# Performance work log

Measured on AMD Instinct MI355X. Metric: run time of the kernel, lower is better.

The kernel has to match this reference:

```python
import jax, jax.numpy as jnp
import numpy as np

# dims: O=1 templates/chains, L=384 residues, d_pair=d_bias=128, 4 heads x 32
O, L, DP, DB, H, DH = 1, 384, 128, 128, 4, 32
SCALING = 1.0 / np.sqrt(DH)


def _ln(x, g, b):
    # torch nn.LayerNorm over last dim, eps=1e-5, biased variance
    m = jnp.mean(x, axis=-1, keepdims=True)
    v = jnp.mean((x - m) ** 2, axis=-1, keepdims=True)
    return (x - m) * jax.lax.rsqrt(v + 1e-5) * g + b


def setup_inputs() -> dict:
    key = jax.random.key(0)
    ks = jax.random.split(key, 9)

    def w(k, shape, s=0.02):
        return (jax.random.normal(k, shape) * s).astype(jnp.float32)

    return {
        "pair": jax.random.normal(ks[0], (O, L, L, DP), dtype=jnp.float32),
        "bias": jax.random.normal(ks[1], (O, L, L, DB), dtype=jnp.float32),
        "ln_pair_g": jnp.ones((DP,), jnp.float32),
        "ln_pair_b": jnp.zeros((DP,), jnp.float32),
        "ln_bias_g": jnp.ones((DB,), jnp.float32),
        "ln_bias_b": jnp.zeros((DB,), jnp.float32),
        "Wq": w(ks[2], (H * DH, DP)),  # torch Linear weight layout (out, in)
        "Wk": w(ks[3], (H * DH, DP)),
        "Wv": w(ks[4], (H * DH, DP)),
        "Wb": w(ks[5], (H, DB)),
        "Wg": w(ks[6], (H * DH, DP)),
        "bg": jnp.ones((H * DH,), jnp.float32),
        "Wo": w(ks[7], (DP, H * DH)),
        "bo": w(ks[8], (DP,)),
    }


def reference(pair, bias, ln_pair_g, ln_pair_b, ln_bias_g, ln_bias_b,
              Wq, Wk, Wv, Wb, Wg, bg, Wo, bo):
    # is_row=True: swap the two L axes so attention runs along rows
    p = jnp.transpose(pair, (0, 2, 1, 3))   # [O, L, L, DP]
    bsrc = jnp.transpose(bias, (0, 2, 1, 3))  # [O, L, L, DB]

    p = _ln(p, ln_pair_g, ln_pair_b)
    bsrc = _ln(bsrc, ln_bias_g, ln_bias_b)

    q = (p @ Wq.T).reshape(O, L, L, H, DH) * SCALING
    k = (p @ Wk.T).reshape(O, L, L, H, DH) / L
    v = (p @ Wv.T).reshape(O, L, L, H, DH)
    b = bsrc @ Wb.T                         # [O, L, L, H] pairwise bias
    gate = jax.nn.sigmoid(p @ Wg.T + bg)    # [O, L, L, H*DH]

    # attention scores contracted over the non-attended axial dim n and head dim k
    attn = jnp.einsum('bnihk,bnjhk->bijh', q, k) + b
    attn = jax.nn.softmax(attn, axis=2)     # softmax over j (torch dim=-2)

    out = jnp.einsum('bijh,bnjhd->bnihd', attn, v).reshape(O, L, L, H * DH)
    out = (gate * out) @ Wo.T + bo          # [O, L, L, DP]
    return jnp.transpose(out, (0, 2, 1, 3))  # undo is_row permute
```

## Files before the change

kernel.cpp:

```cpp
#include <hip/hip_runtime.h>
#include <hip/hip_bf16.h>

#define L_DIM 384
#define DPC 128
#define NH 4
#define DHD 32
#define HD 128
#define NROWS (L_DIM*L_DIM)
#define NSPLIT 16

typedef __hip_bfloat16 bf16;
typedef __attribute__((ext_vector_type(8))) short bf8_t;
typedef __attribute__((ext_vector_type(4))) short bf4_t;
typedef __attribute__((ext_vector_type(4))) float f4_t;

__device__ __forceinline__ float bf2f(bf16 x){ return __bfloat162float(x); }
__device__ __forceinline__ bf16 f2bf(float x){ return __float2bfloat16(x); }

union bfu8 { bf8_t v; bf16 h[8]; };

__global__ __launch_bounds__(256) void k_prep(
    const float* __restrict__ Wq, const float* __restrict__ Wk, const float* __restrict__ Wv,
    const float* __restrict__ Wg, const float* __restrict__ Wo,
    bf16* __restrict__ Wqp, bf16* __restrict__ Wkp, bf16* __restrict__ Wvp,
    bf16* __restrict__ Wgp, bf16* __restrict__ Wop)
{
  const int o = blockIdx.x * 256 + threadIdx.x;
  const int j = o & 7, lane = (o >> 3) & 63, ks = (o >> 9) & 3, nt = o >> 11;
  const int src = (nt*16 + (lane & 15))*DPC + ks*32 + (lane >> 4)*8 + j;
  Wqp[o] = f2bf(Wq[src]);
  Wkp[o] = f2bf(Wk[src]);
  Wvp[o] = f2bf(Wv[src]);
  Wgp[o] = f2bf(Wg[src]);
  Wop[o] = f2bf(Wo[src]);
}

__global__ __launch_bounds__(256) void k_bias_proj(
    const float* __restrict__ bias, const float* __restrict__ lng, const float* __restrict__ lnb,
    const float* __restrict__ Wb, float* __restrict__ bscore)
{
  const int tid = threadIdx.x;
  const int wave = tid >> 6, lane = tid & 63;
  const int sub = lane >> 4, l16 = lane & 15, c = l16 * 8;
  const int t = blockIdx.x * 16 + wave * 4 + sub;
  const int j = t / L_DIM, i = t % L_DIM;

  const float4 ga = *(const float4*)&lng[c], gb = *(const float4*)&lng[c+4];
  const float4 ba = *(const float4*)&lnb[c], bb = *(const float4*)&lnb[c+4];
  const float4 xa = *(const float4*)&bias[(size_t)t * DPC + c];
  const float4 xb = *(const float4*)&bias[(size_t)t * DPC + c + 4];

  float s  = xa.x+xa.y+xa.z+xa.w + xb.x+xb.y+xb.z+xb.w;
  float ss = xa.x*xa.x+xa.y*xa.y+xa.z*xa.z+xa.w*xa.w
           + xb.x*xb.x+xb.y*xb.y+xb.z*xb.z+xb.w*xb.w;
  #pragma unroll
  for (int off = 8; off; off >>= 1) { s += __shfl_xor(s, off, 64); ss += __shfl_xor(ss, off, 64); }
  const float mean = s * (1.f/128.f);
  const float var  = ss * (1.f/128.f) - mean*mean;
  const float rstd = rsqrtf(var + 1e-5f);
  float y[8];
  y[0]=(xa.x-mean)*rstd*ga.x+ba.x; y[1]=(xa.y-mean)*rstd*ga.y+ba.y;
  y[2]=(xa.z-mean)*rstd*ga.z+ba.z; y[3]=(xa.w-mean)*rstd*ga.w+ba.w;
  y[4]=(xb.x-mean)*rstd*gb.x+bb.x; y[5]=(xb.y-mean)*rstd*gb.y+bb.y;
  y[6]=(xb.z-mean)*rstd*gb.z+bb.z; y[7]=(xb.w-mean)*rstd*gb.w+bb.w;

  float p[4];
  #pragma unroll
  for (int h = 0; h < 4; ++h) {
    const float4 wa = *(const float4*)&Wb[h*DPC + c];
    const float4 wb4 = *(const float4*)&Wb[h*DPC + c + 4];
    p[h] = y[0]*wa.x + y[1]*wa.y + y[2]*wa.z + y[3]*wa.w
         + y[4]*wb4.x + y[5]*wb4.y + y[6]*wb4.z + y[7]*wb4.w;
    #pragma unroll
    for (int off = 8; off; off >>= 1) p[h] += __shfl_xor(p[h], off, 64);
  }
  if (l16 == 0) {
    #pragma unroll
    for (int h = 0; h < 4; ++h)
      bscore[((size_t)h*L_DIM + i)*L_DIM + j] = p[h];
  }
}

__global__ __launch_bounds__(256, 6) void k_pair_proj(
    const float* __restrict__ pair, const float* __restrict__ lng, const float* __restrict__ lnb,
    const bf16* __restrict__ Wqp, const bf16* __restrict__ Wkp, const bf16* __restrict__ Wvp,
    const bf16* __restrict__ Wgp, const float* __restrict__ bg,
    bf16* __restrict__ qf, bf16* __restrict__ kf, bf16* __restrict__ vf, bf16* __restrict__ gatef)
{
  __shared__ __align__(16) bf16 Sh[4 * 3072];
  const int tid = threadIdx.x;
  const int wave = tid >> 6, lane = tid & 63;
  bf16* WS = Sh + wave * 3072;
  const int n = blockIdx.x / 6, i6 = blockIdx.x % 6;
  const int i0g = i6*64 + wave*16;
  const int m = lane & 15, q4 = lane >> 4;
  const int I = i6*4 + wave;

  {
    const int half = lane >> 5, l32 = lane & 31, c = l32 * 4;
    const float4 g4 = *(const float4*)&lng[c];
    const float4 b4 = *(const float4*)&lnb[c];
    float4 xv[8];
    #pragma unroll
    for (int rr = 0; rr < 8; ++rr)
      xv[rr] = *(const float4*)&pair[((size_t)(i0g + rr*2 + half)*L_DIM + n)*DPC + c];
    #pragma unroll
    for (int rr = 0; rr < 8; ++rr) {
      const int r = rr*2 + half;
      float s  = xv[rr].x + xv[rr].y + xv[rr].z + xv[rr].w;
      float ss = xv[rr].x*xv[rr].x + xv[rr].y*xv[rr].y + xv[rr].z*xv[rr].z + xv[rr].w*xv[rr].w;
      #pragma unroll
      for (int off = 16; off; off >>= 1) { s += __shfl_xor(s, off, 64); ss += __shfl_xor(ss, off, 64); }
      const float mean = s * (1.f/128.f);
      const float var  = ss * (1.f/128.f) - mean*mean;
      const float rstd = rsqrtf(var + 1e-5f);
      union { bf16 h[4]; bf4_t v; } pk;
      pk.h[0] = f2bf((xv[rr].x-mean)*rstd*g4.x + b4.x);
      pk.h[1] = f2bf((xv[rr].y-mean)*rstd*g4.y + b4.y);
      pk.h[2] = f2bf((xv[rr].z-mean)*rstd*g4.z + b4.z);
      pk.h[3] = f2bf((xv[rr].w-mean)*rstd*g4.w + b4.w);
      *(bf4_t*)&WS[r*136 + c] = pk.v;
    }
  }

  bf8_t afr[4];
  #pragma unroll
  for (int ks = 0; ks < 4; ++ks)
    afr[ks] = *(const bf8_t*)&WS[m*136 + ks*32 + q4*8];

  const bf16* W3[3] = {Wqp, Wkp, Wgp};
  #pragma unroll
  for (int s3 = 0; s3 < 3; ++s3) {
    const bf16* Wp = W3[s3];
    #pragma unroll
    for (int h = 0; h < 4; ++h) {
      f4_t acc0 = {0.f,0.f,0.f,0.f}, acc1 = {0.f,0.f,0.f,0.f};
      #pragma unroll
      for (int ks = 0; ks < 4; ++ks) {
        bf8_t b0 = *(const bf8_t*)&Wp[((h*2    )*4 + ks)*512 + lane*8];
        bf8_t b1 = *(const bf8_t*)&Wp[((h*2 + 1)*4 + ks)*512 + lane*8];
        acc0 = __builtin_amdgcn_mfma_f32_16x16x32_bf16(afr[ks], b0, acc0, 0, 0, 0);
        acc1 = __builtin_amdgcn_mfma_f32_16x16x32_bf16(afr[ks], b1, acc1, 0, 0, 0);
      }
      if (s3 == 2) {
        const float bg0 = bg[h*32 + m], bg1 = bg[h*32 + 16 + m];
        #pragma unroll
        for (int reg = 0; reg < 4; ++reg) {
          acc0[reg] = 1.f / (1.f + __expf(-(acc0[reg] + bg0)));
          acc1[reg] = 1.f / (1.f + __expf(-(acc1[reg] + bg1)));
        }
      }
      #pragma unroll
      for (int reg = 0; reg < 4; ++reg) {
        WS[(q4*4 + reg)*40 + m]      = f2bf(acc0[reg]);
        WS[(q4*4 + reg)*40 + 16 + m] = f2bf(acc1[reg]);
      }
      bf8_t fv = *(const bf8_t*)&WS[m*40 + q4*8];
      if (s3 == 0)
        *(bf8_t*)&qf[((((size_t)n*NH + h)*24 + I)*64 + lane)*8] = fv;
      else if (s3 == 1)
        *(bf8_t*)&kf[((((size_t)n*NH + h)*24 + I)*64 + lane)*8] = fv;
      else
        *(bf8_t*)&gatef[((((size_t)n*24 + I)*NH + h)*64 + lane)*8] = fv;
    }
  }

  #pragma unroll
  for (int nt = 0; nt < 8; ++nt) {
    f4_t acc = {0.f,0.f,0.f,0.f};
    #pragma unroll
    for (int ks = 0; ks < 4; ++ks) {
      bf8_t bfr = *(const bf8_t*)&Wvp[(nt*4 + ks)*512 + lane*8];
      acc = __builtin_amdgcn_mfma_f32_16x16x32_bf16(afr[ks], bfr, acc, 0, 0, 0);
    }
    #pragma unroll
    for (int reg = 0; reg < 4; ++reg)
      WS[(nt*16 + m)*24 + q4*4 + reg] = f2bf(acc[reg]);
  }
  const int J  = i6*2 + (wave >> 1);
  const int wo = (wave & 1) * 32;
  #pragma unroll
  for (int st = 0; st < 4; ++st) {
    const int fid = st*2 + (lane >> 5);
    const int h = fid >> 1, dt = fid & 1;
    const int lnl = lane & 31;
    bf8_t val = *(const bf8_t*)&WS[(h*32 + dt*16 + (lnl & 15))*24 + (lnl >> 4)*8];
    size_t dst = (((((size_t)n*NH + h)*12 + J)*2 + dt)*64 + (wo + lnl))*8;
    *(bf8_t*)&vf[dst] = val;
  }
}

__global__ __launch_bounds__(256) void k_qk(
    const bf16* __restrict__ qf, const bf16* __restrict__ kf, float* __restrict__ Spart)
{
  const int tid = threadIdx.x, wave = tid >> 6, lane = tid & 63;
  const int m = lane & 15, q4 = lane >> 4;
  const int b = blockIdx.x;
  const int ks = b / 36, rem = b % 36;
  const int h = rem / 9, t9 = rem % 9;
  const int i0 = (t9/3)*128, j0 = (t9%3)*128;
  const int wr = (wave >> 1)*64, wc = (wave & 1)*64;

  f4_t acc[4][4];
  #pragma unroll
  for (int a = 0; a < 4; ++a)
    #pragma unroll
    for (int c = 0; c < 4; ++c) acc[a][c] = (f4_t){0.f,0.f,0.f,0.f};

  const bf16* qp = qf + (((size_t)(ks*24)*NH + h)*24 + ((i0 + wr) >> 4))*512 + (size_t)lane*8;
  const bf16* kp = kf + (((size_t)(ks*24)*NH + h)*24 + ((j0 + wc) >> 4))*512 + (size_t)lane*8;
  const size_t nstride = (size_t)NH*24*512;

  bf8_t af[4], bfr[4];
  #pragma unroll
  for (int x = 0; x < 4; ++x) {
    af[x]  = *(const bf8_t*)(qp + x*512);
    bfr[x] = *(const bf8_t*)(kp + x*512);
  }
  #pragma unroll 2
  for (int kt = 0; kt < 24; ++kt) {
    bf8_t afn[4], bfn[4];
    if (kt < 23) {
      const bf16* qn = qp + (size_t)(kt+1)*nstride;
      const bf16* kn = kp + (size_t)(kt+1)*nstride;
      #pragma unroll
      for (int x = 0; x < 4; ++x) {
        afn[x] = *(const bf8_t*)(qn + x*512);
        bfn[x] = *(const bf8_t*)(kn + x*512);
      }
    }
    #pragma unroll
    for (int mt = 0; mt < 4; ++mt)
      #pragma unroll
      for (int nt = 0; nt < 4; ++nt)
        acc[mt][nt] = __builtin_amdgcn_mfma_f32_16x16x32_bf16(af[mt], bfr[nt], acc[mt][nt], 0, 0, 0);
    #pragma unroll
    for (int x = 0; x < 4; ++x) { af[x] = afn[x]; bfr[x] = bfn[x]; }
  }
  float* Sp = Spart + (size_t)(ks*NH + h)*L_DIM*L_DIM;
  #pragma unroll
  for (int mt = 0; mt < 4; ++mt)
    #pragma unroll
    for (int nt = 0; nt < 4; ++nt)
      #pragma unroll
      for (int reg = 0; reg < 4; ++reg) {
        int i = i0 + wr + mt*16 + q4*4 + reg;
        int j = j0 + wc + nt*16 + m;
        Sp[(size_t)i*L_DIM + j] = acc[mt][nt][reg];
      }
}

__global__ __launch_bounds__(192) void k_softmax(
    const float* __restrict__ Spart, const float* __restrict__ bscore, bf16* __restrict__ attnf)
{
  const int t = threadIdx.x, wave = t >> 6, lane = t & 63;
  const int h = blockIdx.x / L_DIM, i = blockIdx.x % L_DIM;
  const float sc = 0.17677669529663687f / 384.f;
  const size_t off = ((size_t)h*L_DIM + i)*L_DIM + t*2;

  float ax = 0.f, ay = 0.f;
  #pragma unroll
  for (int ksp = 0; ksp < NSPLIT; ++ksp) {
    float2 p = *(const float2*)&Spart[(size_t)ksp*(NH*L_DIM*L_DIM) + off];
    ax += p.x; ay += p.y;
  }
  const float2 bs = *(const float2*)&bscore[off];
  ax = ax*sc + bs.x;
  ay = ay*sc + bs.y;

  __shared__ float redm[3], reds[3];
  float mx = fmaxf(ax, ay);
  #pragma unroll
  for (int o = 32; o; o >>= 1) mx = fmaxf(mx, __shfl_xor(mx, o, 64));
  if (lane == 0) redm[wave] = mx;
  __syncthreads();
  mx = fmaxf(fmaxf(redm[0], redm[1]), redm[2]);
  float ex = __expf(ax - mx), ey = __expf(ay - mx);
  float sm = ex + ey;
  #pragma unroll
  for (int o = 32; o; o >>= 1) sm += __shfl_xor(sm, o, 64);
  if (lane == 0) reds[wave] = sm;
  __syncthreads();
  const float inv = 1.f / (reds[0] + reds[1] + reds[2]);

  const int j = t*2;
  const int I = i >> 4, mm = i & 15, J = j >> 5, q4 = (j >> 3) & 3, jj = j & 7;
  union { bf16 h2[2]; unsigned u; } pk;
  pk.h2[0] = f2bf(ex * inv);
  pk.h2[1] = f2bf(ey * inv);
  size_t a = ((((size_t)h*24 + I)*12 + J)*64 + q4*16 + mm)*8 + jj;
  *(unsigned*)&attnf[a] = pk.u;
}

__global__ __launch_bounds__(256) void k_pv(
    const bf16* __restrict__ attnf, const bf16* __restrict__ vf, const bf16* __restrict__ gatef,
    bf16* __restrict__ goutf)
{
  __shared__ __align__(16) bf16 Cs2[384*40];
  const int tid = threadIdx.x, wave = tid >> 6, lane = tid & 63;
  const int m = lane & 15, q4 = lane >> 4;
  const int n = blockIdx.x >> 2, h = blockIdx.x & 3;

  bf8_t ugp[6];
  #pragma unroll
  for (int it = 0; it < 6; ++it) {
    int u = tid + it*256;
    int I = u >> 6, ln = u & 63;
    ugp[it] = *(const bf8_t*)&gatef[((((size_t)n*24 + I)*NH + h)*64 + ln)*8];
  }

  f4_t acc[6][2];
  #pragma unroll
  for (int a = 0; a < 6; ++a) { acc[a][0] = (f4_t){0,0,0,0}; acc[a][1] = (f4_t){0,0,0,0}; }

  for (int J = 0; J < 12; ++J) {
    const bf16* vb = vf + (((size_t)(n*NH + h)*12 + J)*2)*512;
    bf8_t b0 = *(const bf8_t*)&vb[lane*8];
    bf8_t b1 = *(const bf8_t*)&vb[512 + lane*8];
    #pragma unroll
    for (int mt = 0; mt < 6; ++mt) {
      const int I = wave*6 + mt;
      bf8_t af = *(const bf8_t*)&attnf[(((size_t)h*24 + I)*12 + J)*512 + (size_t)lane*8];
      acc[mt][0] = __builtin_amdgcn_mfma_f32_16x16x32_bf16(af, b0, acc[mt][0], 0, 0, 0);
      acc[mt][1] = __builtin_amdgcn_mfma_f32_16x16x32_bf16(af, b1, acc[mt][1], 0, 0, 0);
    }
  }
  #pragma unroll
  for (int mt = 0; mt < 6; ++mt)
    #pragma unroll
    for (int dt = 0; dt < 2; ++dt)
      #pragma unroll
      for (int reg = 0; reg < 4; ++reg) {
        int i_loc = 16*(wave*6 + mt) + q4*4 + reg;
        Cs2[i_loc*40 + dt*16 + m] = f2bf(acc[mt][dt][reg]);
      }
  __syncthreads();
  #pragma unroll
  for (int it = 0; it < 6; ++it) {
    int u = tid + it*256;
    int I = u >> 6, ln = u & 63;
    bfu8 uc, ug, uo;
    uc.v = *(const bf8_t*)&Cs2[(I*16 + (ln&15))*40 + (ln>>4)*8];
    ug.v = ugp[it];
    #pragma unroll
    for (int e = 0; e < 8; ++e) uo.h[e] = f2bf(bf2f(uc.h[e]) * bf2f(ug.h[e]));
    size_t gidx = ((((size_t)n*24 + I)*NH + h)*64 + ln)*8;
    *(bf8_t*)&goutf[gidx] = uo.v;
  }
}

__global__ __launch_bounds__(256) void k_out(
    const bf16* __restrict__ goutf, const bf16* __restrict__ Wop, const float* __restrict__ bo,
    float* __restrict__ outp)
{
  __shared__ __align__(16) float Cs[64][132];
  const int tid = threadIdx.x, wave = tid >> 6, lane = tid & 63;
  const int m = lane & 15, q4 = lane >> 4;
  const int n = blockIdx.x / 6, i0 = (blockIdx.x % 6) * 64;

  bf8_t afr[4];
  #pragma unroll
  for (int ks = 0; ks < 4; ++ks)
    afr[ks] = *(const bf8_t*)&goutf[((((size_t)n*24 + (i0>>4) + wave)*NH + ks)*64 + lane)*8];

  #pragma unroll
  for (int nt = 0; nt < 8; ++nt) {
    f4_t acc = {0.f, 0.f, 0.f, 0.f};
    #pragma unroll
    for (int ks = 0; ks < 4; ++ks) {
      bf8_t bfr = *(const bf8_t*)&Wop[(nt*4 + ks)*512 + lane*8];
      acc = __builtin_amdgcn_mfma_f32_16x16x32_bf16(afr[ks], bfr, acc, 0, 0, 0);
    }
    const int col = nt*16 + m;
    const float bov = bo[col];
    #pragma unroll
    for (int reg = 0; reg < 4; ++reg)
      Cs[wave*16 + q4*4 + reg][col] = acc[reg] + bov;
  }
  __syncthreads();
  for (int u = tid; u < 2048; u += 256) {
    int r = u >> 5, c4 = (u & 31) * 4;
    size_t off = ((size_t)(i0 + r)*L_DIM + n)*DPC + c4;
    *(float4*)&outp[off] = *(const float4*)&Cs[r][c4];
  }
}

extern "C" void kernel_launch(void* const* d_in, const int* in_sizes, int n_in,
                              void* d_out, int out_size, void* d_ws, size_t ws_size,
                              hipStream_t stream)
{
  (void)in_sizes; (void)n_in; (void)out_size; (void)ws_size;
  const float* pair = (const float*)d_in[0];
  const float* bias = (const float*)d_in[1];
  const float* lnpg = (const float*)d_in[2];
  const float* lnpb = (const float*)d_in[3];
  const float* lnbg = (const float*)d_in[4];
  const float* lnbb = (const float*)d_in[5];
  const float* Wq   = (const float*)d_in[6];
  const float* Wk   = (const float*)d_in[7];
  const float* Wv   = (const float*)d_in[8];
  const float* Wb   = (const float*)d_in[9];
  const float* Wg   = (const float*)d_in[10];
  const float* bg   = (const float*)d_in[11];
  const float* Wo   = (const float*)d_in[12];
  const float* bo   = (const float*)d_in[13];
  float* outp = (float*)d_out;

  char* ws = (char*)d_ws;
  const size_t SZ = (size_t)NROWS * HD * 2;
  bf16* qfb   = (bf16*)(ws);
  bf16* kfb   = (bf16*)(ws + SZ);
  bf16* vfb   = (bf16*)(ws + 2*SZ);
  bf16* gatef = (bf16*)(ws + 3*SZ);
  float* bscore = (float*)(ws + 4*SZ);
  float* Spart  = (float*)(ws + 4*SZ + (size_t)NH*L_DIM*L_DIM*4);
  bf16*  attnf  = (bf16*)(ws + 4*SZ + (size_t)NH*L_DIM*L_DIM*4 + (size_t)NSPLIT*NH*L_DIM*L_DIM*4);
  char*  wb     = ws + 4*SZ + (size_t)NH*L_DIM*L_DIM*4 + (size_t)NSPLIT*NH*L_DIM*L_DIM*4
                     + (size_t)NH*L_DIM*L_DIM*2;
  bf16* Wqp = (bf16*)(wb);
  bf16* Wkp = (bf16*)(wb + 32768);
  bf16* Wvp = (bf16*)(wb + 65536);
  bf16* Wgp = (bf16*)(wb + 98304);
  bf16* Wop = (bf16*)(wb + 131072);
  bf16* goutf = qfb;

  hipLaunchKernelGGL(k_prep, dim3(64), dim3(256), 0, stream, Wq, Wk, Wv, Wg, Wo,
                     Wqp, Wkp, Wvp, Wgp, Wop);
  hipLaunchKernelGGL(k_bias_proj, dim3(NROWS/16), dim3(256), 0, stream, bias, lnbg, lnbb, Wb, bscore);
  hipLaunchKernelGGL(k_pair_proj, dim3(NROWS/64), dim3(256), 0, stream, pair, lnpg, lnpb,
                     Wqp, Wkp, Wvp, Wgp, bg, qfb, kfb, vfb, gatef);
  hipLaunchKernelGGL(k_qk, dim3(NSPLIT*36), dim3(256), 0, stream, qfb, kfb, Spart);
  hipLaunchKernelGGL(k_softmax, dim3(NH*L_DIM), dim3(192), 0, stream, Spart, bscore, attnf);
  hipLaunchKernelGGL(k_pv, dim3(L_DIM*NH), dim3(256), 0, stream, attnf, vfb, gatef, goutf);
  hipLaunchKernelGGL(k_out, dim3(NROWS/64), dim3(256), 0, stream, goutf, Wop, bo, outp);
}
```

Before: 392.2 us.

## Interleave Q, K, gate and V projections into one block-contiguous workspace buffer

k_pair_proj now writes Q, K, gate and V for each (n, 64-row block) into one contiguous 64KB chunk instead of four separate strided arrays. The aim is fully contiguous write bursts from the projection kernel, and reads in k_pv that stay local for gate and V. It changes the read strides in k_qk and k_pv. The gated output buffer now reuses the Spart region instead of the Q buffer. The risk is larger strides and less contiguous access for the Q/K loads in k_qk.

Result: slower. 400.3 us (+2.1%).

```diff
diff --git a/kernel.cpp b/kernel.cpp
--- a/kernel.cpp
+++ b/kernel.cpp
@@ -8,6 +8,12 @@
 #define HD 128
 #define NROWS (L_DIM*L_DIM)
 #define NSPLIT 16
+
+#define SB_BF16 32768
+#define SB_Q 0
+#define SB_K 8192
+#define SB_G 16384
+#define SB_V 24576
 
 typedef __hip_bfloat16 bf16;
 typedef __attribute__((ext_vector_type(8))) short bf8_t;
@@ -85,7 +91,7 @@
     const float* __restrict__ pair, const float* __restrict__ lng, const float* __restrict__ lnb,
     const bf16* __restrict__ Wqp, const bf16* __restrict__ Wkp, const bf16* __restrict__ Wvp,
     const bf16* __restrict__ Wgp, const float* __restrict__ bg,
-    bf16* __restrict__ qf, bf16* __restrict__ kf, bf16* __restrict__ vf, bf16* __restrict__ gatef)
+    bf16* __restrict__ fused)
 {
   __shared__ __align__(16) bf16 Sh[4 * 3072];
   const int tid = threadIdx.x;
@@ -94,7 +100,8 @@
   const int n = blockIdx.x / 6, i6 = blockIdx.x % 6;
   const int i0g = i6*64 + wave*16;
   const int m = lane & 15, q4 = lane >> 4;
-  const int I = i6*4 + wave;
+
+  bf16* SB = fused + ((size_t)n*6 + i6) * SB_BF16;
 
   {
     const int half = lane >> 5, l32 = lane & 31, c = l32 * 4;
@@ -129,6 +136,7 @@
     afr[ks] = *(const bf8_t*)&WS[m*136 + ks*32 + q4*8];
 
   const bf16* W3[3] = {Wqp, Wkp, Wgp};
+  const int soff3[3] = {SB_Q, SB_K, SB_G};
   #pragma unroll
   for (int s3 = 0; s3 < 3; ++s3) {
     const bf16* Wp = W3[s3];
@@ -156,12 +164,7 @@
         WS[(q4*4 + reg)*40 + 16 + m] = f2bf(acc1[reg]);
       }
       bf8_t fv = *(const bf8_t*)&WS[m*40 + q4*8];
-      if (s3 == 0)
-        *(bf8_t*)&qf[((((size_t)n*NH + h)*24 + I)*64 + lane)*8] = fv;
-      else if (s3 == 1)
-        *(bf8_t*)&kf[((((size_t)n*NH + h)*24 + I)*64 + lane)*8] = fv;
-      else
-        *(bf8_t*)&gatef[((((size_t)n*24 + I)*NH + h)*64 + lane)*8] = fv;
+      *(bf8_t*)&SB[soff3[s3] + (h*4 + wave)*512 + lane*8] = fv;
     }
   }
 
@@ -177,7 +180,7 @@
     for (int reg = 0; reg < 4; ++reg)
       WS[(nt*16 + m)*24 + q4*4 + reg] = f2bf(acc[reg]);
   }
-  const int J  = i6*2 + (wave >> 1);
+  const int Jloc = wave >> 1;
   const int wo = (wave & 1) * 32;
   #pragma unroll
   for (int st = 0; st < 4; ++st) {
@@ -185,13 +188,12 @@
     const int h = fid >> 1, dt = fid & 1;
     const int lnl = lane & 31;
     bf8_t val = *(const bf8_t*)&WS[(h*32 + dt*16 + (lnl & 15))*24 + (lnl >> 4)*8];
-    size_t dst = (((((size_t)n*NH + h)*12 + J)*2 + dt)*64 + (wo + lnl))*8;
-    *(bf8_t*)&vf[dst] = val;
+    *(bf8_t*)&SB[SB_V + (((Jloc*4 + h)*2 + dt)*512) + (wo + lnl)*8] = val;
   }
 }
 
 __global__ __launch_bounds__(256) void k_qk(
-    const bf16* __restrict__ qf, const bf16* __restrict__ kf, float* __restrict__ Spart)
+    const bf16* __restrict__ fused, float* __restrict__ Spart)
 {
   const int tid = threadIdx.x, wave = tid >> 6, lane = tid & 63;
   const int m = lane & 15, q4 = lane >> 4;
@@ -207,9 +209,11 @@
     #pragma unroll
     for (int c = 0; c < 4; ++c) acc[a][c] = (f4_t){0.f,0.f,0.f,0.f};
 
-  const bf16* qp = qf + (((size_t)(ks*24)*NH + h)*24 + ((i0 + wr) >> 4))*512 + (size_t)lane*8;
-  const bf16* kp = kf + (((size_t)(ks*24)*NH + h)*24 + ((j0 + wc) >> 4))*512 + (size_t)lane*8;
-  const size_t nstride = (size_t)NH*24*512;
+  const bf16* qp = fused + ((size_t)(ks*24)*6 + ((i0 + wr) >> 6))*SB_BF16
+                         + SB_Q + h*2048 + (size_t)lane*8;
+  const bf16* kp = fused + ((size_t)(ks*24)*6 + ((j0 + wc) >> 6))*SB_BF16
+                         + SB_K + h*2048 + (size_t)lane*8;
+  const size_t nstride = (size_t)6*SB_BF16;
 
   bf8_t af[4], bfr[4];
   #pragma unroll
@@ -293,7 +297,7 @@
 }
 
 __global__ __launch_bounds__(256) void k_pv(
-    const bf16* __restrict__ attnf, const bf16* __restrict__ vf, const bf16* __restrict__ gatef,
+    const bf16* __restrict__ attnf, const bf16* __restrict__ fused,
     bf16* __restrict__ goutf)
 {
   __shared__ __align__(16) bf16 Cs2[384*40];
@@ -306,7 +310,8 @@
   for (int it = 0; it < 6; ++it) {
     int u = tid + it*256;
     int I = u >> 6, ln = u & 63;
-    ugp[it] = *(const bf8_t*)&gatef[((((size_t)n*24 + I)*NH + h)*64 + ln)*8];
+    ugp[it] = *(const bf8_t*)&fused[((size_t)n*6 + (I>>2))*SB_BF16 + SB_G
+                                    + (h*4 + (I&3))*512 + ln*8];
   }
 
   f4_t acc[6][2];
@@ -314,7 +319,8 @@
   for (int a = 0; a < 6; ++a) { acc[a][0] = (f4_t){0,0,0,0}; acc[a][1] = (f4_t){0,0,0,0}; }
 
   for (int J = 0; J < 12; ++J) {
-    const bf16* vb = vf + (((size_t)(n*NH + h)*12 + J)*2)*512;
+    const bf16* vb = fused + ((size_t)n*6 + (J>>1))*SB_BF16 + SB_V
+                           + (((J&1)*4 + h)*2)*512;
     bf8_t b0 = *(const bf8_t*)&vb[lane*8];
     bf8_t b1 = *(const bf8_t*)&vb[512 + lane*8];
     #pragma unroll
@@ -407,30 +413,28 @@
   float* outp = (float*)d_out;
 
   char* ws = (char*)d_ws;
-  const size_t SZ = (size_t)NROWS * HD * 2;
-  bf16* qfb   = (bf16*)(ws);
-  bf16* kfb   = (bf16*)(ws + SZ);
-  bf16* vfb   = (bf16*)(ws + 2*SZ);
-  bf16* gatef = (bf16*)(ws + 3*SZ);
-  float* bscore = (float*)(ws + 4*SZ);
-  float* Spart  = (float*)(ws + 4*SZ + (size_t)NH*L_DIM*L_DIM*4);
-  bf16*  attnf  = (bf16*)(ws + 4*SZ + (size_t)NH*L_DIM*L_DIM*4 + (size_t)NSPLIT*NH*L_DIM*L_DIM*4);
-  char*  wb     = ws + 4*SZ + (size_t)NH*L_DIM*L_DIM*4 + (size_t)NSPLIT*NH*L_DIM*L_DIM*4
-                     + (size_t)NH*L_DIM*L_DIM*2;
+  const size_t FUSED_SZ = (size_t)2304 * SB_BF16 * 2;
+  bf16* fusedb  = (bf16*)(ws);
+  float* bscore = (float*)(ws + FUSED_SZ);
+  float* Spart  = (float*)(ws + FUSED_SZ + (size_t)NH*L_DIM*L_DIM*4);
+  bf16*  attnf  = (bf16*)(ws + FUSED_SZ + (size_t)NH*L_DIM*L_DIM*4
+                             + (size_t)NSPLIT*NH*L_DIM*L_DIM*4);
+  char*  wb     = ws + FUSED_SZ + (size_t)NH*L_DIM*L_DIM*4
+                     + (size_t)NSPLIT*NH*L_DIM*L_DIM*4 + (size_t)NH*L_DIM*L_DIM*2;
   bf16* Wqp = (bf16*)(wb);
   bf16* Wkp = (bf16*)(wb + 32768);
   bf16* Wvp = (bf16*)(wb + 65536);
   bf16* Wgp = (bf16*)(wb + 98304);
   bf16* Wop = (bf16*)(wb + 131072);
-  bf16* goutf = qfb;
+  bf16* goutf = (bf16*)Spart;
 
   hipLaunchKernelGGL(k_prep, dim3(64), dim3(256), 0, stream, Wq, Wk, Wv, Wg, Wo,
                      Wqp, Wkp, Wvp, Wgp, Wop);
   hipLaunchKernelGGL(k_bias_proj, dim3(NROWS/16), dim3(256), 0, stream, bias, lnbg, lnbb, Wb, bscore);
   hipLaunchKernelGGL(k_pair_proj, dim3(NROWS/64), dim3(256), 0, stream, pair, lnpg, lnpb,
-                     Wqp, Wkp, Wvp, Wgp, bg, qfb, kfb, vfb, gatef);
-  hipLaunchKernelGGL(k_qk, dim3(NSPLIT*36), dim3(256), 0, stream, qfb, kfb, Spart);
+                     Wqp, Wkp, Wvp, Wgp, bg, fusedb);
+  hipLaunchKernelGGL(k_qk, dim3(NSPLIT*36), dim3(256), 0, stream, fusedb, Spart);
   hipLaunchKernelGGL(k_softmax, dim3(NH*L_DIM), dim3(192), 0, stream, Spart, bscore, attnf);
-  hipLaunchKernelGGL(k_pv, dim3(L_DIM*NH), dim3(256), 0, stream, attnf, vfb, gatef, goutf);
+  hipLaunchKernelGGL(k_pv, dim3(L_DIM*NH), dim3(256), 0, stream, attnf, fusedb, goutf);
   hipLaunchKernelGGL(k_out, dim3(NROWS/64), dim3(256), 0, stream, goutf, Wop, bo, outp);
 }
```
